# Kernel optimization log

Measured on AMD Instinct MI355X. Metric: run time of the kernel, lower is better.

Reference implementation:

```python
import jax, jax.numpy as jnp
import numpy as np

NUM_CLASSES = 2
IGNORE_INDEX = 2


def setup_inputs() -> dict:
    key = jax.random.key(0)
    k1, k2 = jax.random.split(key)
    probs = jax.random.uniform(k1, (2, 2, 32, 512, 512), dtype=jnp.float32)  # (B,C,D,H,W)
    gt_mask = jax.random.randint(k2, (2, 32, 512, 512), 0, 3, dtype=jnp.int32)  # (B,D,H,W), includes ignore_index=2
    return {"probs": probs, "gt_mask": gt_mask}


def _one_hot_target(gt_mask):
    # ignore_index -> 0, clamp to [0, NUM_CLASSES-1], one-hot to channel axis 1
    gt = jnp.where(gt_mask == IGNORE_INDEX, 0, gt_mask)
    gt = jnp.clip(gt, 0, NUM_CLASSES - 1)
    oh = jax.nn.one_hot(gt, NUM_CLASSES, dtype=jnp.float32)  # (B,D,H,W,C)
    return jnp.moveaxis(oh, -1, 1)  # (B,C,D,H,W)


def reference(probs, gt_mask):
    # Per-z-slice 2D loss (surrogate for the opaque topological _loss_2d:
    # mean squared error between probs and one-hot target per slice),
    # vectorized over the z loop, then 'mean' reduction over slices.
    oh = _one_hot_target(gt_mask)  # (B,C,D,H,W)
    per_z = jnp.mean((probs - oh) ** 2, axis=(0, 1, 3, 4))  # (D,)
    return jnp.mean(per_z)
```

## Files before the change

### kernel.cpp

```cpp
#include <hip/hip_runtime.h>

static constexpr long long DHW       = 32LL * 512 * 512;
static constexpr long long N_SPATIAL = 2LL * DHW;
static constexpr long long N_TOTAL   = 2LL * N_SPATIAL;

__global__ __launch_bounds__(256) void betti_mse_reduce(const float* __restrict__ probs,
                                                        const int*   __restrict__ mask,
                                                        double*      __restrict__ acc) {
    const long long nvec   = N_SPATIAL / 4;
    const long long stride = (long long)gridDim.x * blockDim.x;
    float local = 0.0f;

    for (long long v = (long long)blockIdx.x * blockDim.x + threadIdx.x; v < nvec; v += stride) {
        const long long s    = v << 2;
        const long long b    = s >> 23;
        const long long rest = s & (DHW - 1);
        const long long base = (b << 24) + rest;

        const float4 p0 = *reinterpret_cast<const float4*>(probs + base);
        const float4 p1 = *reinterpret_cast<const float4*>(probs + base + DHW);
        const int4   m  = *reinterpret_cast<const int4*>(mask + s);

        const float t0 = (m.x == 1) ? 1.0f : 0.0f;
        const float t1 = (m.y == 1) ? 1.0f : 0.0f;
        const float t2 = (m.z == 1) ? 1.0f : 0.0f;
        const float t3 = (m.w == 1) ? 1.0f : 0.0f;

        float d;
        d = p0.x - (1.0f - t0); local += d * d;
        d = p0.y - (1.0f - t1); local += d * d;
        d = p0.z - (1.0f - t2); local += d * d;
        d = p0.w - (1.0f - t3); local += d * d;
        d = p1.x - t0;          local += d * d;
        d = p1.y - t1;          local += d * d;
        d = p1.z - t2;          local += d * d;
        d = p1.w - t3;          local += d * d;
    }

    #pragma unroll
    for (int off = 32; off > 0; off >>= 1)
        local += __shfl_down(local, off, 64);

    __shared__ float wsum[4];
    const int lane = threadIdx.x & 63;
    const int wid  = threadIdx.x >> 6;
    if (lane == 0) wsum[wid] = local;
    __syncthreads();
    if (threadIdx.x == 0) {
        const float blocksum = wsum[0] + wsum[1] + wsum[2] + wsum[3];
        atomicAdd(acc, (double)blocksum);
    }
}

__global__ void betti_finalize(const double* __restrict__ acc, float* __restrict__ out) {
    out[0] = (float)(acc[0] / (double)N_TOTAL);
}

extern "C" void kernel_launch(void* const* d_in, const int* in_sizes, int n_in,
                              void* d_out, int out_size, void* d_ws, size_t ws_size,
                              hipStream_t stream) {
    const float* probs = (const float*)d_in[0];
    const int*   mask  = (const int*)d_in[1];
    float*       out   = (float*)d_out;
    double*      acc   = (double*)d_ws;

    hipMemsetAsync(acc, 0, sizeof(double), stream);

    const int block = 256;
    const int grid  = 4096;
    betti_mse_reduce<<<grid, block, 0, stream>>>(probs, mask, acc);
    betti_finalize<<<1, 1, 0, stream>>>(acc, out);
}
```

Measured before the change: 238.9 us.

## Replace atomic reduction with per-block partials and a fixed unrolled loop

The grid-stride loop becomes a fully unrolled loop of exactly 8 iterations per thread, split across two independent accumulators so more loads are in flight. The double atomicAdd and the memset launch are replaced by per-block partial sums written to the workspace, which a single-block kernel then reduces. The aim is more memory-level parallelism and one less launch, plus no atomic contention. In exchange the kernel is tied to the exact input size through a static_assert, and the grid drops to 2048 blocks.

```diff
diff --git a/kernel.cpp b/kernel.cpp
--- a/kernel.cpp
+++ b/kernel.cpp
@@ -4,38 +4,52 @@
 static constexpr long long N_SPATIAL = 2LL * DHW;
 static constexpr long long N_TOTAL   = 2LL * N_SPATIAL;
 
-__global__ __launch_bounds__(256) void betti_mse_reduce(const float* __restrict__ probs,
-                                                        const int*   __restrict__ mask,
-                                                        double*      __restrict__ acc) {
-    const long long nvec   = N_SPATIAL / 4;
-    const long long stride = (long long)gridDim.x * blockDim.x;
-    float local = 0.0f;
+static constexpr int GRID  = 2048;
+static constexpr int BLOCK = 256;
+static constexpr long long NVEC   = N_SPATIAL / 4;
+static constexpr long long STRIDE = (long long)GRID * BLOCK;
+static_assert(NVEC == 8 * STRIDE, "exact 8 iterations per thread");
 
-    for (long long v = (long long)blockIdx.x * blockDim.x + threadIdx.x; v < nvec; v += stride) {
-        const long long s    = v << 2;
-        const long long b    = s >> 23;
-        const long long rest = s & (DHW - 1);
-        const long long base = (b << 24) + rest;
+__device__ __forceinline__ float chunk_mse(const float* __restrict__ probs,
+                                           const int*   __restrict__ mask,
+                                           long long v) {
+    const long long s    = v << 2;
+    const long long b    = s >> 23;
+    const long long rest = s & (DHW - 1);
+    const long long base = (b << 24) + rest;
 
-        const float4 p0 = *reinterpret_cast<const float4*>(probs + base);
-        const float4 p1 = *reinterpret_cast<const float4*>(probs + base + DHW);
-        const int4   m  = *reinterpret_cast<const int4*>(mask + s);
+    const float4 p0 = *reinterpret_cast<const float4*>(probs + base);
+    const float4 p1 = *reinterpret_cast<const float4*>(probs + base + DHW);
+    const int4   m  = *reinterpret_cast<const int4*>(mask + s);
 
-        const float t0 = (m.x == 1) ? 1.0f : 0.0f;
-        const float t1 = (m.y == 1) ? 1.0f : 0.0f;
-        const float t2 = (m.z == 1) ? 1.0f : 0.0f;
-        const float t3 = (m.w == 1) ? 1.0f : 0.0f;
+    const float t0 = (m.x == 1) ? 1.0f : 0.0f;
+    const float t1 = (m.y == 1) ? 1.0f : 0.0f;
+    const float t2 = (m.z == 1) ? 1.0f : 0.0f;
+    const float t3 = (m.w == 1) ? 1.0f : 0.0f;
 
-        float d;
-        d = p0.x - (1.0f - t0); local += d * d;
-        d = p0.y - (1.0f - t1); local += d * d;
-        d = p0.z - (1.0f - t2); local += d * d;
-        d = p0.w - (1.0f - t3); local += d * d;
-        d = p1.x - t0;          local += d * d;
-        d = p1.y - t1;          local += d * d;
-        d = p1.z - t2;          local += d * d;
-        d = p1.w - t3;          local += d * d;
+    float acc = 0.0f, d;
+    d = p0.x - (1.0f - t0); acc += d * d;
+    d = p0.y - (1.0f - t1); acc += d * d;
+    d = p0.z - (1.0f - t2); acc += d * d;
+    d = p0.w - (1.0f - t3); acc += d * d;
+    d = p1.x - t0;          acc += d * d;
+    d = p1.y - t1;          acc += d * d;
+    d = p1.z - t2;          acc += d * d;
+    d = p1.w - t3;          acc += d * d;
+    return acc;
+}
+
+__global__ __launch_bounds__(BLOCK) void betti_mse_partial(const float* __restrict__ probs,
+                                                           const int*   __restrict__ mask,
+                                                           double*      __restrict__ partial) {
+    const long long v0 = (long long)blockIdx.x * BLOCK + threadIdx.x;
+    float acc0 = 0.0f, acc1 = 0.0f;
+    #pragma unroll
+    for (int i = 0; i < 4; ++i) {
+        acc0 += chunk_mse(probs, mask, v0 + (2 * i + 0) * STRIDE);
+        acc1 += chunk_mse(probs, mask, v0 + (2 * i + 1) * STRIDE);
     }
+    float local = acc0 + acc1;
 
     #pragma unroll
     for (int off = 32; off > 0; off >>= 1)
@@ -46,28 +60,38 @@
     const int wid  = threadIdx.x >> 6;
     if (lane == 0) wsum[wid] = local;
     __syncthreads();
-    if (threadIdx.x == 0) {
-        const float blocksum = wsum[0] + wsum[1] + wsum[2] + wsum[3];
-        atomicAdd(acc, (double)blocksum);
-    }
+    if (threadIdx.x == 0)
+        partial[blockIdx.x] = (double)(wsum[0] + wsum[1] + wsum[2] + wsum[3]);
 }
 
-__global__ void betti_finalize(const double* __restrict__ acc, float* __restrict__ out) {
-    out[0] = (float)(acc[0] / (double)N_TOTAL);
+__global__ __launch_bounds__(BLOCK) void betti_mse_final(const double* __restrict__ partial,
+                                                         float* __restrict__ out) {
+    double local = 0.0;
+    #pragma unroll
+    for (int k = 0; k < GRID / BLOCK; ++k)
+        local += partial[threadIdx.x + k * BLOCK];
+
+    #pragma unroll
+    for (int off = 32; off > 0; off >>= 1)
+        local += __shfl_down(local, off, 64);
+
+    __shared__ double wsum[4];
+    const int lane = threadIdx.x & 63;
+    const int wid  = threadIdx.x >> 6;
+    if (lane == 0) wsum[wid] = local;
+    __syncthreads();
+    if (threadIdx.x == 0)
+        out[0] = (float)((wsum[0] + wsum[1] + wsum[2] + wsum[3]) / (double)N_TOTAL);
 }
 
 extern "C" void kernel_launch(void* const* d_in, const int* in_sizes, int n_in,
                               void* d_out, int out_size, void* d_ws, size_t ws_size,
                               hipStream_t stream) {
-    const float* probs = (const float*)d_in[0];
-    const int*   mask  = (const int*)d_in[1];
-    float*       out   = (float*)d_out;
-    double*      acc   = (double*)d_ws;
+    const float* probs   = (const float*)d_in[0];
+    const int*   mask    = (const int*)d_in[1];
+    float*       out     = (float*)d_out;
+    double*      partial = (double*)d_ws;
 
-    hipMemsetAsync(acc, 0, sizeof(double), stream);
-
-    const int block = 256;
-    const int grid  = 4096;
-    betti_mse_reduce<<<grid, block, 0, stream>>>(probs, mask, acc);
-    betti_finalize<<<1, 1, 0, stream>>>(acc, out);
+    betti_mse_partial<<<GRID, BLOCK, 0, stream>>>(probs, mask, partial);
+    betti_mse_final<<<1, BLOCK, 0, stream>>>(partial, out);
 }
```

Measured after the change: 234.1 us. 2.0% less time.
